# Optimization experiments

Measured on AMD Instinct MI355X. Metric: run time of the kernel, lower is better.

Reference implementation:

```python
import jax, jax.numpy as jnp
import numpy as np

D_MODEL = 1024
NHEAD = 16
HEAD_DIM = D_MODEL // NHEAD
NEG = -1e9
LN_EPS = 1e-5


def setup_inputs() -> dict:
    key = jax.random.key(0)
    ks = jax.random.split(key, 12)
    B, S, D = 2, 2048, D_MODEL
    scale = 1.0 / np.sqrt(D)
    inp = {
        "x": jax.random.normal(ks[0], (B, S, D), jnp.float32),
        "mask": jax.random.randint(ks[1], (B, S), 0, 2, jnp.int32),
        "wq": jax.random.normal(ks[2], (D, D), jnp.float32) * scale,
        "bq": jnp.zeros((D,), jnp.float32),
        "wk": jax.random.normal(ks[3], (D, D), jnp.float32) * scale,
        "bk": jnp.zeros((D,), jnp.float32),
        "wv": jax.random.normal(ks[4], (D, D), jnp.float32) * scale,
        "bv": jnp.zeros((D,), jnp.float32),
        "wo": jax.random.normal(ks[5], (D, D), jnp.float32) * scale,
        "bo": jnp.zeros((D,), jnp.float32),
        "attn_bias": jax.random.normal(ks[6], (1, NHEAD, 1, 1), jnp.float32) * 0.02,
        "ln_g": jnp.ones((D,), jnp.float32),
        "ln_b": jnp.zeros((D,), jnp.float32),
    }
    return inp


def _layer_norm(x, g, b):
    mu = jnp.mean(x, axis=-1, keepdims=True)
    var = jnp.var(x, axis=-1, keepdims=True)
    return (x - mu) * jax.lax.rsqrt(var + LN_EPS) * g + b


def reference(x, mask, wq, bq, wk, bk, wv, bv, wo, bo, attn_bias, ln_g, ln_b):
    B, S, D = x.shape
    H, Hd = NHEAD, HEAD_DIM
    # QKV projections -> [B, H, S, Hd]
    q = (x @ wq + bq).reshape(B, S, H, Hd).transpose(0, 2, 1, 3)
    k = (x @ wk + bk).reshape(B, S, H, Hd).transpose(0, 2, 1, 3)
    v = (x @ wv + bv).reshape(B, S, H, Hd).transpose(0, 2, 1, 3)
    # Scores [B, H, S, S] with per-head scalar bias
    scores = jnp.einsum("bhsd,bhtd->bhst", q, k) / jnp.sqrt(jnp.float32(Hd))
    scores = scores + attn_bias
    # mask [B,S] -> [B,1,1,S]; masked_fill where mask == 0
    m = (mask[:, None, None, :] == 0)
    scores = jnp.where(m, jnp.float32(NEG), scores)
    attn = jax.nn.softmax(scores, axis=-1)  # dropout = identity (eval)
    out = jnp.einsum("bhst,bhtd->bhsd", attn, v)
    out = out.transpose(0, 2, 1, 3).reshape(B, S, D)
    out = out @ wo + bo
    return _layer_norm(x + out, ln_g, ln_b)
```

## Files before the change

### kernel.cpp

```cpp
#include <hip/hip_runtime.h>

typedef __attribute__((ext_vector_type(8))) short short8;
typedef __attribute__((ext_vector_type(4))) float f32x4;
typedef __attribute__((ext_vector_type(16))) float f32x16;
typedef __attribute__((ext_vector_type(4))) unsigned short us4;

#define DEV __device__ __forceinline__

#define GLD16(gp, lp) __builtin_amdgcn_global_load_lds( \
    (const __attribute__((address_space(1))) void*)(gp), \
    (__attribute__((address_space(3))) void*)(lp), 16, 0, 0)

DEV unsigned short f2bf(float f) {
    union { float f; unsigned u; } v; v.f = f;
    unsigned r = v.u + 0x7fffu + ((v.u >> 16) & 1u);
    return (unsigned short)(r >> 16);
}

DEV float bf2f(unsigned short u) {
    union { unsigned u; float f; } v; v.u = (unsigned)u << 16;
    return v.f;
}

DEV unsigned short f2h(float f) {
    union { _Float16 h; unsigned short u; } v; v.h = (_Float16)f; return v.u;
}

DEV float h2f(unsigned short u) {
    union { _Float16 h; unsigned short u; } v; v.u = u; return (float)v.h;
}

DEV unsigned cvtpk(float lo, float hi) {
    unsigned r;
    asm("v_cvt_pk_bf16_f32 %0, %1, %2" : "=v"(r) : "v"(lo), "v"(hi));
    return r;
}

DEV float fexp2(float x) {
#if __has_builtin(__builtin_amdgcn_exp2f)
    return __builtin_amdgcn_exp2f(x);
#else
    return __expf(x * 0.69314718056f);
#endif
}

__global__ __launch_bounds__(256) void k_convert(const float* __restrict__ x,
                                                 unsigned short* __restrict__ xb) {
    int i = blockIdx.x * 256 + threadIdx.x;
    float4 v = ((const float4*)x)[i];
    us4 o = { f2bf(v.x), f2bf(v.y), f2bf(v.z), f2bf(v.w) };
    ((us4*)xb)[i] = o;
}

__global__ __launch_bounds__(256) void k_transw(const float* __restrict__ wq, const float* __restrict__ wk,
                                                const float* __restrict__ wv, const float* __restrict__ wo,
                                                unsigned short* __restrict__ wt) {
    __shared__ float tile[32][33];
    const int z = blockIdx.z;
    const float* src = (z == 0) ? wq : (z == 1) ? wk : (z == 2) ? wv : wo;
    unsigned short* dst = wt + (size_t)z * (1u << 20);
    const int n0 = blockIdx.x * 32, k0 = blockIdx.y * 32;
    const int tx = threadIdx.x, ty = threadIdx.y;
#pragma unroll
    for (int i = 0; i < 4; ++i)
        tile[ty + i * 8][tx] = src[(size_t)(k0 + ty + i * 8) * 1024 + n0 + tx];
    __syncthreads();
#pragma unroll
    for (int i = 0; i < 4; ++i)
        dst[(size_t)(n0 + ty + i * 8) * 1024 + k0 + tx] = f2bf(tile[tx][ty + i * 8]);
}

__global__ __launch_bounds__(256) void k_gemm_qkv(const unsigned short* __restrict__ A,
                                                  const unsigned short* __restrict__ Wt,
                                                  const float* __restrict__ bq,
                                                  const float* __restrict__ bk,
                                                  const float* __restrict__ bv,
                                                  const int* __restrict__ mask,
                                                  unsigned short* __restrict__ Qo,
                                                  unsigned short* __restrict__ Ko,
                                                  unsigned short* __restrict__ Vo,
                                                  float qscale) {
    __shared__ unsigned short lA[2][128 * 32];
    __shared__ unsigned short lB[2][3][64 * 32];
    const int id = blockIdx.x;
    const int m0 = ((id & 7) * 4 + ((id >> 3) & 3)) * 128;
    const int n0 = (id >> 5) * 64;
    const int tid = threadIdx.x;
    const int lane = tid & 63;
    const int w = tid >> 6, wm = w >> 1, wn = w & 1;

    const int arow0 = tid >> 2, acl = tid & 3;
    const int arow1 = (tid + 256) >> 2;
    const int brow = tid >> 2;
    const unsigned short* agp0 = A + (size_t)(m0 + arow0) * 1024 + acl * 8;
    const unsigned short* agp1 = A + (size_t)(m0 + arow1) * 1024 + acl * 8;
    const unsigned short* bgp[3];
#pragma unroll
    for (int z = 0; z < 3; ++z)
        bgp[z] = Wt + ((size_t)z << 20) + (size_t)(n0 + brow) * 1024 + acl * 8;
    const int apc0 = ((arow0 << 2) | (acl ^ ((arow0 >> 1) & 3))) * 8;
    const int apc1 = ((arow1 << 2) | (acl ^ ((arow1 >> 1) & 3))) * 8;
    const int bpc  = ((brow  << 2) | (acl ^ ((brow  >> 1) & 3))) * 8;

    int ach[4], bch[2];
#pragma unroll
    for (int mt = 0; mt < 4; ++mt) {
        int row = wm * 64 + mt * 16 + (lane & 15);
        ach[mt] = ((row << 2) | ((lane >> 4) ^ ((row >> 1) & 3))) * 8;
    }
#pragma unroll
    for (int nt = 0; nt < 2; ++nt) {
        int row = wn * 32 + nt * 16 + (lane & 15);
        bch[nt] = ((row << 2) | ((lane >> 4) ^ ((row >> 1) & 3))) * 8;
    }

    f32x4 acc[3][4][2] = {};
    short8 ra0 = *(const short8*)agp0;
    short8 ra1 = *(const short8*)agp1;
    short8 rb[3];
#pragma unroll
    for (int z = 0; z < 3; ++z) rb[z] = *(const short8*)bgp[z];

    for (int t = 0; t < 32; ++t) {
        unsigned short* sA = lA[t & 1];
        *(short8*)(sA + apc0) = ra0;
        *(short8*)(sA + apc1) = ra1;
#pragma unroll
        for (int z = 0; z < 3; ++z)
            *(short8*)(lB[t & 1][z] + bpc) = rb[z];
        if (t < 31) {
            ra0 = *(const short8*)(agp0 + (t + 1) * 32);
            ra1 = *(const short8*)(agp1 + (t + 1) * 32);
#pragma unroll
            for (int z = 0; z < 3; ++z) rb[z] = *(const short8*)(bgp[z] + (t + 1) * 32);
        }
        __syncthreads();
        short8 af[4], bf[3][2];
#pragma unroll
        for (int mt = 0; mt < 4; ++mt) af[mt] = *(const short8*)(sA + ach[mt]);
#pragma unroll
        for (int z = 0; z < 3; ++z)
#pragma unroll
            for (int nt = 0; nt < 2; ++nt) bf[z][nt] = *(const short8*)(lB[t & 1][z] + bch[nt]);
#pragma unroll
        for (int z = 0; z < 3; ++z)
#pragma unroll
            for (int mt = 0; mt < 4; ++mt)
#pragma unroll
                for (int nt = 0; nt < 2; ++nt)
                    acc[z][mt][nt] = __builtin_amdgcn_mfma_f32_16x16x32_bf16(af[mt], bf[z][nt], acc[z][mt][nt], 0, 0, 0);
    }

#pragma unroll
    for (int z = 0; z < 3; ++z) {
        const float* bias = (z == 0) ? bq : (z == 1) ? bk : bv;
        const float scl = (z == 0) ? qscale : 1.0f;
        unsigned short* outp = (z == 0) ? Qo : (z == 1) ? Ko : Vo;
#pragma unroll
        for (int nt = 0; nt < 2; ++nt) {
            const int col = n0 + wn * 32 + nt * 16 + (lane & 15);
            const float bvv = bias[col];
            const int h = col >> 6, hd = col & 63;
#pragma unroll
            for (int mt = 0; mt < 4; ++mt) {
#pragma unroll
                for (int r = 0; r < 4; ++r) {
                    const int row = m0 + wm * 64 + mt * 16 + (lane >> 4) * 4 + r;
                    const int b = row >> 11, s = row & 2047;
                    float v = (acc[z][mt][nt][r] + bvv) * scl;
                    if (z == 2) {
                        v *= (mask[(size_t)b * 2048 + s] ? 1.0f : 0.0f);
                        outp[(size_t)((b * 16 + h) * 64 + hd) * 2048 + s] = f2bf(v);
                    } else {
                        outp[(size_t)((b * 16 + h) * 2048 + s) * 64 + hd] = f2bf(v);
                    }
                }
            }
        }
    }
}

__global__ __launch_bounds__(256) void k_gemm_o(const unsigned short* __restrict__ A,
                                                const unsigned short* __restrict__ Wt,
                                                const float* __restrict__ bias,
                                                unsigned short* __restrict__ out) {
    __shared__ unsigned short lA[2][128 * 32];
    __shared__ unsigned short lB[2][64 * 32];
    const int id = blockIdx.x;
    const int m0 = ((id & 7) * 4 + ((id >> 3) & 3)) * 128;
    const int n0 = (id >> 5) * 64;
    const int tid = threadIdx.x;
    const int lane = tid & 63;
    const int w = tid >> 6, wm = w >> 1, wn = w & 1;

    const int arow0 = tid >> 2, acl = tid & 3;
    const int arow1 = (tid + 256) >> 2;
    const int brow = tid >> 2;
    const unsigned short* agp0 = A + (size_t)(m0 + arow0) * 1024 + acl * 8;
    const unsigned short* agp1 = A + (size_t)(m0 + arow1) * 1024 + acl * 8;
    const unsigned short* bgp  = Wt + (size_t)(n0 + brow) * 1024 + acl * 8;
    const int apc0 = ((arow0 << 2) | (acl ^ ((arow0 >> 1) & 3))) * 8;
    const int apc1 = ((arow1 << 2) | (acl ^ ((arow1 >> 1) & 3))) * 8;
    const int bpc  = ((brow  << 2) | (acl ^ ((brow  >> 1) & 3))) * 8;

    int ach[4], bch[2];
#pragma unroll
    for (int mt = 0; mt < 4; ++mt) {
        int row = wm * 64 + mt * 16 + (lane & 15);
        ach[mt] = ((row << 2) | ((lane >> 4) ^ ((row >> 1) & 3))) * 8;
    }
#pragma unroll
    for (int nt = 0; nt < 2; ++nt) {
        int row = wn * 32 + nt * 16 + (lane & 15);
        bch[nt] = ((row << 2) | ((lane >> 4) ^ ((row >> 1) & 3))) * 8;
    }

    f32x4 acc[4][2] = {};
    short8 ra0 = *(const short8*)agp0;
    short8 ra1 = *(const short8*)agp1;
    short8 rb0 = *(const short8*)bgp;

    for (int t = 0; t < 32; ++t) {
        unsigned short* sA = lA[t & 1];
        unsigned short* sB = lB[t & 1];
        *(short8*)(sA + apc0) = ra0;
        *(short8*)(sA + apc1) = ra1;
        *(short8*)(sB + bpc)  = rb0;
        if (t < 31) {
            ra0 = *(const short8*)(agp0 + (t + 1) * 32);
            ra1 = *(const short8*)(agp1 + (t + 1) * 32);
            rb0 = *(const short8*)(bgp  + (t + 1) * 32);
        }
        __syncthreads();
        short8 af[4], bf[2];
#pragma unroll
        for (int mt = 0; mt < 4; ++mt) af[mt] = *(const short8*)(sA + ach[mt]);
#pragma unroll
        for (int nt = 0; nt < 2; ++nt) bf[nt] = *(const short8*)(sB + bch[nt]);
#pragma unroll
        for (int mt = 0; mt < 4; ++mt)
#pragma unroll
            for (int nt = 0; nt < 2; ++nt)
                acc[mt][nt] = __builtin_amdgcn_mfma_f32_16x16x32_bf16(af[mt], bf[nt], acc[mt][nt], 0, 0, 0);
    }

#pragma unroll
    for (int nt = 0; nt < 2; ++nt) {
        const int col = n0 + wn * 32 + nt * 16 + (lane & 15);
        const float bv = bias[col];
#pragma unroll
        for (int mt = 0; mt < 4; ++mt)
#pragma unroll
            for (int r = 0; r < 4; ++r) {
                const int row = m0 + wm * 64 + mt * 16 + (lane >> 4) * 4 + r;
                out[(size_t)row * 1024 + col] = f2bf(acc[mt][nt][r] + bv);
            }
    }
}

__global__ __launch_bounds__(256, 4) void k_attn(const unsigned short* __restrict__ Qb,
                                                 const unsigned short* __restrict__ Kb,
                                                 const unsigned short* __restrict__ Vt,
                                                 const int* __restrict__ mask,
                                                 unsigned short* __restrict__ po0,
                                                 unsigned short* __restrict__ po1,
                                                 unsigned short* __restrict__ po2,
                                                 unsigned short* __restrict__ po3,
                                                 float* __restrict__ lp) {
    __shared__ unsigned short ksm[2 * 4096];
    __shared__ unsigned short vsm[2 * 4096];
    __shared__ unsigned short mv[512];
    const int id = blockIdx.x;
    const int xcd = id & 7, slot = id >> 3;
    const int half = slot & 3, qt = (slot >> 2) & 15, bh = xcd * 4 + (slot >> 6);
    const int b = bh >> 4, h = bh & 15;
    const int tid = threadIdx.x, l = tid & 63, w = tid >> 6;
    const int q = l & 31, hi = l >> 5;

    {
        int2 m = ((const int2*)(mask + b * 2048 + half * 512))[tid];
        ((unsigned*)mv)[tid] = (m.x ? 0x3F80u : 0u) | ((m.y ? 0x3F80u : 0u) << 16);
    }
    asm volatile("s_waitcnt lgkmcnt(0)" ::: "memory");

    const size_t bhS = (size_t)bh * 2048;
    const unsigned short* Kbh = Kb + (bhS + half * 512) * 64;
    const unsigned short* Vbh = Vt + (size_t)bh * 64 * 2048;
    const int q0 = qt * 128 + w * 32;

    const int srow = l >> 3;
    const int sxor = 8 * ((l & 7) ^ ((l >> 3) & 7));
    const unsigned short* Ksrc = Kbh + (size_t)(w * 16 + srow) * 64 + sxor;
    const unsigned short* Vsrc = Vbh + (size_t)(w * 16 + srow) * 2048 + half * 512 + sxor;
    unsigned short* lk0 = ksm + w * 1024;
    unsigned short* lv0 = vsm + w * 1024;

#define STAGE(kt_, buf_) { \
    const unsigned short* gk = Ksrc + (size_t)(kt_) * 4096; \
    const unsigned short* gv = Vsrc + (kt_) * 64; \
    unsigned short* lk = lk0 + (buf_) * 4096; \
    unsigned short* lv = lv0 + (buf_) * 4096; \
    GLD16(gk, lk); GLD16(gk + 512, lk + 512); \
    GLD16(gv, lv); GLD16(gv + 16384, lv + 512); }

    int kro[2][4], vro[2][2][2];
#pragma unroll
    for (int sub = 0; sub < 2; ++sub) {
#pragma unroll
        for (int db = 0; db < 4; ++db) {
            int key = q + sub * 32;
            kro[sub][db] = key * 128 + ((db * 32 + hi * 16) ^ ((key & 7) << 4));
        }
#pragma unroll
        for (int kg = 0; kg < 2; ++kg)
#pragma unroll
            for (int dh = 0; dh < 2; ++dh) {
                int row = q + dh * 32;
                vro[sub][kg][dh] = row * 128 + ((sub * 64 + kg * 32 + hi * 16) ^ ((row & 7) << 4));
            }
    }

    short8 qf[4];
#pragma unroll
    for (int db = 0; db < 4; ++db)
        qf[db] = *(const short8*)(Qb + (bhS + q0 + q) * 64 + db * 16 + hi * 8);

    f32x16 o0 = {}, o1 = {}, ol = {};

    STAGE(0, 0);

    for (int kt = 0; kt < 8; ++kt) {
        const int cur = kt & 1;
        if (kt < 7) {
            STAGE(kt + 1, cur ^ 1);
            asm volatile("s_waitcnt vmcnt(4)" ::: "memory");
        } else {
            asm volatile("s_waitcnt vmcnt(0)" ::: "memory");
        }
        __builtin_amdgcn_s_barrier();
        __builtin_amdgcn_sched_barrier(0);
        const char* kb = (const char*)(ksm + cur * 4096);
        const char* vb = (const char*)(vsm + cur * 4096);
#pragma unroll
        for (int sub = 0; sub < 2; ++sub) {
            short8 kf0 = *(const short8*)(kb + kro[sub][0]);
            short8 kf1 = *(const short8*)(kb + kro[sub][1]);
            short8 kf2 = *(const short8*)(kb + kro[sub][2]);
            short8 kf3 = *(const short8*)(kb + kro[sub][3]);
            f32x16 sa = {};
            __builtin_amdgcn_s_setprio(1);
            sa = __builtin_amdgcn_mfma_f32_32x32x16_bf16(kf0, qf[0], sa, 0, 0, 0);
            sa = __builtin_amdgcn_mfma_f32_32x32x16_bf16(kf1, qf[1], sa, 0, 0, 0);
            sa = __builtin_amdgcn_mfma_f32_32x32x16_bf16(kf2, qf[2], sa, 0, 0, 0);
            sa = __builtin_amdgcn_mfma_f32_32x32x16_bf16(kf3, qf[3], sa, 0, 0, 0);
            __builtin_amdgcn_s_setprio(0);
            float p[16];
#pragma unroll
            for (int r = 0; r < 16; ++r) p[r] = fexp2(sa[r]);
            union { unsigned u[4]; short8 s8; } af[2];
#pragma unroll
            for (int kg = 0; kg < 2; ++kg) {
                unsigned P0 = cvtpk(p[kg * 8 + 0], p[kg * 8 + 1]);
                unsigned P1 = cvtpk(p[kg * 8 + 2], p[kg * 8 + 3]);
                unsigned P2 = cvtpk(p[kg * 8 + 4], p[kg * 8 + 5]);
                unsigned P3 = cvtpk(p[kg * 8 + 6], p[kg * 8 + 7]);
                asm("v_permlane32_swap_b32 %0, %1" : "+v"(P0), "+v"(P2));
                asm("v_permlane32_swap_b32 %0, %1" : "+v"(P1), "+v"(P3));
                af[kg].u[0] = P0; af[kg].u[1] = P1; af[kg].u[2] = P2; af[kg].u[3] = P3;
            }
#pragma unroll
            for (int kg = 0; kg < 2; ++kg) {
                short8 vf0 = *(const short8*)(vb + vro[sub][kg][0]);
                short8 vf1 = *(const short8*)(vb + vro[sub][kg][1]);
                short8 mfr = *(const short8*)(mv + kt * 64 + sub * 32 + kg * 16 + hi * 8);
                __builtin_amdgcn_s_setprio(1);
                o0 = __builtin_amdgcn_mfma_f32_32x32x16_bf16(af[kg].s8, vf0, o0, 0, 0, 0);
                o1 = __builtin_amdgcn_mfma_f32_32x32x16_bf16(af[kg].s8, vf1, o1, 0, 0, 0);
                ol = __builtin_amdgcn_mfma_f32_32x32x16_bf16(af[kg].s8, mfr, ol, 0, 0, 0);
                __builtin_amdgcn_s_setprio(0);
            }
        }
        __builtin_amdgcn_sched_barrier(0);
        if (kt < 7) __builtin_amdgcn_s_barrier();
    }
#undef STAGE

    float* lpx = lp + (size_t)half * 65536 + bhS;
    if (q == 0) {
#pragma unroll
        for (int r = 0; r < 16; ++r) {
            int crow = (r & 3) + 8 * (r >> 2) + 4 * hi;
            lpx[q0 + crow] = ol[r];
        }
    }
    unsigned short* pox = (half == 0) ? po0 : (half == 1) ? po1 : (half == 2) ? po2 : po3;
    unsigned short* pop = pox + ((size_t)b * 2048 + q0) * 1024 + h * 64 + q;
#pragma unroll
    for (int r = 0; r < 16; ++r) {
        int qrow = (r & 3) + 8 * (r >> 2) + 4 * hi;
        pop[(size_t)qrow * 1024] = f2h(o0[r]);
        pop[(size_t)qrow * 1024 + 32] = f2h(o1[r]);
    }
}

__global__ __launch_bounds__(256) void k_comb(const unsigned short* __restrict__ po0,
                                              const unsigned short* __restrict__ po1,
                                              const unsigned short* __restrict__ po2,
                                              const unsigned short* __restrict__ po3,
                                              const float* __restrict__ lp,
                                              unsigned short* __restrict__ ao) {
    const int idx8 = blockIdx.x * 256 + threadIdx.x;
    const int e = idx8 * 8;
    const int row = e >> 10, c = e & 1023;
    const int h = c >> 6, b = row >> 11, s = row & 2047;
    const size_t li = ((size_t)(b * 16 + h) << 11) + s;
    const float lsum = lp[li] + lp[65536 + li] + lp[2 * 65536 + li] + lp[3 * 65536 + li];
    const float rinv = __builtin_amdgcn_rcpf(lsum);
    short8 a0 = ((const short8*)po0)[idx8];
    short8 a1 = ((const short8*)po1)[idx8];
    short8 a2 = ((const short8*)po2)[idx8];
    short8 a3 = ((const short8*)po3)[idx8];
    short8 o;
#pragma unroll
    for (int j = 0; j < 8; ++j) {
        float s4 = (h2f((unsigned short)a0[j]) + h2f((unsigned short)a1[j]))
                 + (h2f((unsigned short)a2[j]) + h2f((unsigned short)a3[j]));
        o[j] = (short)f2bf(s4 * rinv);
    }
    ((short8*)ao)[idx8] = o;
}

__global__ __launch_bounds__(256) void k_ln(const float* __restrict__ x, const unsigned short* __restrict__ op,
                                            const float* __restrict__ g, const float* __restrict__ be,
                                            float* __restrict__ out) {
    const int row = blockIdx.x, tid = threadIdx.x;
    const float4 xv = ((const float4*)(x + (size_t)row * 1024))[tid];
    const us4 ov = ((const us4*)(op + (size_t)row * 1024))[tid];
    float4 v = { xv.x + bf2f(ov.x), xv.y + bf2f(ov.y), xv.z + bf2f(ov.z), xv.w + bf2f(ov.w) };
    float sum = v.x + v.y + v.z + v.w;
    float ss = v.x * v.x + v.y * v.y + v.z * v.z + v.w * v.w;
#pragma unroll
    for (int xm = 1; xm < 64; xm <<= 1) {
        sum += __shfl_xor(sum, xm, 64);
        ss += __shfl_xor(ss, xm, 64);
    }
    __shared__ float red[8];
    const int lane = tid & 63, w = tid >> 6;
    if (lane == 0) { red[w] = sum; red[4 + w] = ss; }
    __syncthreads();
    sum = red[0] + red[1] + red[2] + red[3];
    ss = red[4] + red[5] + red[6] + red[7];
    const float mu = sum * (1.0f / 1024.0f);
    const float rstd = rsqrtf(ss * (1.0f / 1024.0f) - mu * mu + 1e-5f);
    const float4 gv = ((const float4*)g)[tid];
    const float4 bv = ((const float4*)be)[tid];
    float4 o = { (v.x - mu) * rstd * gv.x + bv.x, (v.y - mu) * rstd * gv.y + bv.y,
                 (v.z - mu) * rstd * gv.z + bv.z, (v.w - mu) * rstd * gv.w + bv.w };
    ((float4*)(out + (size_t)row * 1024))[tid] = o;
}

extern "C" void kernel_launch(void* const* d_in, const int* in_sizes, int n_in,
                              void* d_out, int out_size, void* d_ws, size_t ws_size,
                              hipStream_t stream) {
    const float* x        = (const float*)d_in[0];
    const int*   mask     = (const int*)d_in[1];
    const float* wq       = (const float*)d_in[2];
    const float* bq       = (const float*)d_in[3];
    const float* wk       = (const float*)d_in[4];
    const float* bk       = (const float*)d_in[5];
    const float* wv       = (const float*)d_in[6];
    const float* bv       = (const float*)d_in[7];
    const float* wo       = (const float*)d_in[8];
    const float* bo       = (const float*)d_in[9];
    const float* ln_g     = (const float*)d_in[11];
    const float* ln_b     = (const float*)d_in[12];

    char* ws = (char*)d_ws;
    unsigned short* xb  = (unsigned short*)(ws);
    unsigned short* wt  = (unsigned short*)(ws + (8ll  << 20));
    unsigned short* qb  = (unsigned short*)(ws + (16ll << 20));
    unsigned short* kb  = (unsigned short*)(ws + (24ll << 20));
    unsigned short* vtb = (unsigned short*)(ws + (32ll << 20));
    unsigned short* po1 = (unsigned short*)(ws + (40ll << 20));
    float*          lp  = (float*)(ws + (48ll << 20));
    unsigned short* po0 = xb;
    unsigned short* po2 = (unsigned short*)d_out;
    unsigned short* po3 = po2 + (4ll << 20);
    unsigned short* ao  = qb;
    unsigned short* opj = kb;

    const float qscale = 0.125f * 1.44269504f;

    k_convert<<<4096, 256, 0, stream>>>(x, xb);
    k_transw<<<dim3(32, 32, 4), dim3(32, 8), 0, stream>>>(wq, wk, wv, wo, wt);
    k_gemm_qkv<<<512, 256, 0, stream>>>(xb, wt, bq, bk, bv, mask, qb, kb, vtb, qscale);
    k_attn<<<2048, 256, 0, stream>>>(qb, kb, vtb, mask, po0, po1, po2, po3, lp);
    k_comb<<<2048, 256, 0, stream>>>(po0, po1, po2, po3, lp, ao);
    k_gemm_o<<<512, 256, 0, stream>>>(ao, wt + (3u << 20), bo, opj);
    k_ln<<<4096, 256, 0, stream>>>(x, opj, ln_g, ln_b, (float*)d_out);
}
```

Before: 132.2 us.

## Merge prep kernels, enlarge O-proj tile, triple-buffer attention K/V staging

Fuses the x conversion and weight transpose into a single launch to save one kernel launch. Widens the output-projection GEMM tile from 128x64 to 128x128, halving the grid and raising reuse of the A tile. Switches the attention kernel to a three-stage K/V shared-memory ring that prefetches two tiles ahead and drops the trailing barrier. The extra LDS lowers the occupancy target from 4 to 3 blocks per CU, and the vmcnt(4) wait count may no longer match the number of loads in flight.

```diff
diff --git a/kernel.cpp b/kernel.cpp
--- a/kernel.cpp
+++ b/kernel.cpp
@@ -44,23 +44,24 @@
 #endif
 }
 
-__global__ __launch_bounds__(256) void k_convert(const float* __restrict__ x,
-                                                 unsigned short* __restrict__ xb) {
-    int i = blockIdx.x * 256 + threadIdx.x;
-    float4 v = ((const float4*)x)[i];
-    us4 o = { f2bf(v.x), f2bf(v.y), f2bf(v.z), f2bf(v.w) };
-    ((us4*)xb)[i] = o;
-}
-
-__global__ __launch_bounds__(256) void k_transw(const float* __restrict__ wq, const float* __restrict__ wk,
-                                                const float* __restrict__ wv, const float* __restrict__ wo,
-                                                unsigned short* __restrict__ wt) {
+__global__ __launch_bounds__(256) void k_prep(const float* __restrict__ x, unsigned short* __restrict__ xb,
+                                              const float* __restrict__ wq, const float* __restrict__ wk,
+                                              const float* __restrict__ wv, const float* __restrict__ wo,
+                                              unsigned short* __restrict__ wt) {
     __shared__ float tile[32][33];
-    const int z = blockIdx.z;
+    const int id = blockIdx.x, tid = threadIdx.x;
+    if (id < 4096) {
+        int i = id * 256 + tid;
+        float4 v = ((const float4*)x)[i];
+        us4 o = { f2bf(v.x), f2bf(v.y), f2bf(v.z), f2bf(v.w) };
+        ((us4*)xb)[i] = o;
+        return;
+    }
+    const int t = (id - 4096) & 1023, z = (id - 4096) >> 10;
     const float* src = (z == 0) ? wq : (z == 1) ? wk : (z == 2) ? wv : wo;
     unsigned short* dst = wt + (size_t)z * (1u << 20);
-    const int n0 = blockIdx.x * 32, k0 = blockIdx.y * 32;
-    const int tx = threadIdx.x, ty = threadIdx.y;
+    const int n0 = (t & 31) * 32, k0 = (t >> 5) * 32;
+    const int tx = tid & 31, ty = tid >> 5;
 #pragma unroll
     for (int i = 0; i < 4; ++i)
         tile[ty + i * 8][tx] = src[(size_t)(k0 + ty + i * 8) * 1024 + n0 + tx];
@@ -185,68 +186,71 @@
                                                 const float* __restrict__ bias,
                                                 unsigned short* __restrict__ out) {
     __shared__ unsigned short lA[2][128 * 32];
-    __shared__ unsigned short lB[2][64 * 32];
+    __shared__ unsigned short lB[2][128 * 32];
     const int id = blockIdx.x;
-    const int m0 = ((id & 7) * 4 + ((id >> 3) & 3)) * 128;
-    const int n0 = (id >> 5) * 64;
+    const int kk = id >> 3;
+    const int m0 = ((id & 7) * 4 + (kk >> 3)) * 128;
+    const int n0 = (kk & 7) * 128;
     const int tid = threadIdx.x;
     const int lane = tid & 63;
     const int w = tid >> 6, wm = w >> 1, wn = w & 1;
 
     const int arow0 = tid >> 2, acl = tid & 3;
-    const int arow1 = (tid + 256) >> 2;
-    const int brow = tid >> 2;
+    const int arow1 = arow0 + 64;
     const unsigned short* agp0 = A + (size_t)(m0 + arow0) * 1024 + acl * 8;
     const unsigned short* agp1 = A + (size_t)(m0 + arow1) * 1024 + acl * 8;
-    const unsigned short* bgp  = Wt + (size_t)(n0 + brow) * 1024 + acl * 8;
+    const unsigned short* bgp0 = Wt + (size_t)(n0 + arow0) * 1024 + acl * 8;
+    const unsigned short* bgp1 = Wt + (size_t)(n0 + arow1) * 1024 + acl * 8;
     const int apc0 = ((arow0 << 2) | (acl ^ ((arow0 >> 1) & 3))) * 8;
     const int apc1 = ((arow1 << 2) | (acl ^ ((arow1 >> 1) & 3))) * 8;
-    const int bpc  = ((brow  << 2) | (acl ^ ((brow  >> 1) & 3))) * 8;
-
-    int ach[4], bch[2];
+
+    int ach[4], bch[4];
 #pragma unroll
     for (int mt = 0; mt < 4; ++mt) {
         int row = wm * 64 + mt * 16 + (lane & 15);
         ach[mt] = ((row << 2) | ((lane >> 4) ^ ((row >> 1) & 3))) * 8;
     }
 #pragma unroll
-    for (int nt = 0; nt < 2; ++nt) {
-        int row = wn * 32 + nt * 16 + (lane & 15);
+    for (int nt = 0; nt < 4; ++nt) {
+        int row = wn * 64 + nt * 16 + (lane & 15);
         bch[nt] = ((row << 2) | ((lane >> 4) ^ ((row >> 1) & 3))) * 8;
     }
 
-    f32x4 acc[4][2] = {};
+    f32x4 acc[4][4] = {};
     short8 ra0 = *(const short8*)agp0;
     short8 ra1 = *(const short8*)agp1;
-    short8 rb0 = *(const short8*)bgp;
+    short8 rb0 = *(const short8*)bgp0;
+    short8 rb1 = *(const short8*)bgp1;
 
     for (int t = 0; t < 32; ++t) {
         unsigned short* sA = lA[t & 1];
         unsigned short* sB = lB[t & 1];
         *(short8*)(sA + apc0) = ra0;
         *(short8*)(sA + apc1) = ra1;
-        *(short8*)(sB + bpc)  = rb0;
+        *(short8*)(sB + apc0) = rb0;
+        *(short8*)(sB + apc1) = rb1;
         if (t < 31) {
             ra0 = *(const short8*)(agp0 + (t + 1) * 32);
             ra1 = *(const short8*)(agp1 + (t + 1) * 32);
-            rb0 = *(const short8*)(bgp  + (t + 1) * 32);
+            rb0 = *(const short8*)(bgp0 + (t + 1) * 32);
+            rb1 = *(const short8*)(bgp1 + (t + 1) * 32);
         }
         __syncthreads();
-        short8 af[4], bf[2];
+        short8 af[4], bf[4];
 #pragma unroll
         for (int mt = 0; mt < 4; ++mt) af[mt] = *(const short8*)(sA + ach[mt]);
 #pragma unroll
-        for (int nt = 0; nt < 2; ++nt) bf[nt] = *(const short8*)(sB + bch[nt]);
+        for (int nt = 0; nt < 4; ++nt) bf[nt] = *(const short8*)(sB + bch[nt]);
 #pragma unroll
         for (int mt = 0; mt < 4; ++mt)
 #pragma unroll
-            for (int nt = 0; nt < 2; ++nt)
+            for (int nt = 0; nt < 4; ++nt)
                 acc[mt][nt] = __builtin_amdgcn_mfma_f32_16x16x32_bf16(af[mt], bf[nt], acc[mt][nt], 0, 0, 0);
     }
 
 #pragma unroll
-    for (int nt = 0; nt < 2; ++nt) {
-        const int col = n0 + wn * 32 + nt * 16 + (lane & 15);
+    for (int nt = 0; nt < 4; ++nt) {
+        const int col = n0 + wn * 64 + nt * 16 + (lane & 15);
         const float bv = bias[col];
 #pragma unroll
         for (int mt = 0; mt < 4; ++mt)
@@ -258,7 +262,7 @@
     }
 }
 
-__global__ __launch_bounds__(256, 4) void k_attn(const unsigned short* __restrict__ Qb,
+__global__ __launch_bounds__(256, 3) void k_attn(const unsigned short* __restrict__ Qb,
                                                  const unsigned short* __restrict__ Kb,
                                                  const unsigned short* __restrict__ Vt,
                                                  const int* __restrict__ mask,
@@ -267,8 +271,8 @@
                                                  unsigned short* __restrict__ po2,
                                                  unsigned short* __restrict__ po3,
                                                  float* __restrict__ lp) {
-    __shared__ unsigned short ksm[2 * 4096];
-    __shared__ unsigned short vsm[2 * 4096];
+    __shared__ unsigned short ksm[3 * 4096];
+    __shared__ unsigned short vsm[3 * 4096];
     __shared__ unsigned short mv[512];
     const int id = blockIdx.x;
     const int xcd = id & 7, slot = id >> 3;
@@ -328,16 +332,18 @@
     f32x16 o0 = {}, o1 = {}, ol = {};
 
     STAGE(0, 0);
-
+    STAGE(1, 1);
+
+#pragma unroll
     for (int kt = 0; kt < 8; ++kt) {
-        const int cur = kt & 1;
+        const int cur = kt % 3;
         if (kt < 7) {
-            STAGE(kt + 1, cur ^ 1);
             asm volatile("s_waitcnt vmcnt(4)" ::: "memory");
         } else {
             asm volatile("s_waitcnt vmcnt(0)" ::: "memory");
         }
         __builtin_amdgcn_s_barrier();
+        if (kt < 6) STAGE(kt + 2, (kt + 2) % 3);
         __builtin_amdgcn_sched_barrier(0);
         const char* kb = (const char*)(ksm + cur * 4096);
         const char* vb = (const char*)(vsm + cur * 4096);
@@ -381,7 +387,6 @@
             }
         }
         __builtin_amdgcn_sched_barrier(0);
-        if (kt < 7) __builtin_amdgcn_s_barrier();
     }
 #undef STAGE
 
@@ -491,11 +496,10 @@
 
     const float qscale = 0.125f * 1.44269504f;
 
-    k_convert<<<4096, 256, 0, stream>>>(x, xb);
-    k_transw<<<dim3(32, 32, 4), dim3(32, 8), 0, stream>>>(wq, wk, wv, wo, wt);
+    k_prep<<<8192, 256, 0, stream>>>(x, xb, wq, wk, wv, wo, wt);
     k_gemm_qkv<<<512, 256, 0, stream>>>(xb, wt, bq, bk, bv, mask, qb, kb, vtb, qscale);
     k_attn<<<2048, 256, 0, stream>>>(qb, kb, vtb, mask, po0, po1, po2, po3, lp);
     k_comb<<<2048, 256, 0, stream>>>(po0, po1, po2, po3, lp, ao);
-    k_gemm_o<<<512, 256, 0, stream>>>(ao, wt + (3u << 20), bo, opj);
+    k_gemm_o<<<256, 256, 0, stream>>>(ao, wt + (3u << 20), bo, opj);
     k_ln<<<4096, 256, 0, stream>>>(x, opj, ln_g, ln_b, (float*)d_out);
 }
```

Measured after the change: 130.0 us. Within noise of the previous version (-1.6%).
